# Optimization experiments

Hardware: AMD Instinct MI355X
Metric: run time of the kernel (lower is better)

Reference implementation:

```python
import jax, jax.numpy as jnp
import numpy as np

SCALE = 100.0
ALPHA_MEM = 0.9
ALPHA_MEM_OUT = 0.9
ALPHA_R = 0.85
ALPHA_X = 0.95
ALPHA_P = 0.95
ALPHA_D = 0.95
WMIN = 0.0
WMAX = 2.0


@jax.custom_vjp
def spike_fn(x):
    # SurrGradSpike.forward: heaviside(x)
    return (x > 0).astype(x.dtype)

def _spike_fwd(x):
    return spike_fn(x), x

def _spike_bwd(x, g):
    # SurrGradSpike.backward: g / (scale*|x| + 1)^2
    return (g / (SCALE * jnp.abs(x) + 1.0) ** 2,)

spike_fn.defvjp(_spike_fwd, _spike_bwd)


def setup_inputs() -> dict:
    key = jax.random.key(0)
    ks = jax.random.split(key, 8)
    B, T, NI, N, NO, D = 8, 64, 256, 512, 32, 4
    inputs = jax.random.normal(ks[0], (B, T, NI), jnp.float32)
    w = jax.random.normal(ks[1], (N, N), jnp.float32) * (0.1 / np.sqrt(N))
    w_in = jax.random.normal(ks[2], (NI, N), jnp.float32) * (1.0 / np.sqrt(NI))
    w_out = jax.random.normal(ks[3], (N, NO), jnp.float32) * (1.0 / np.sqrt(N))
    # each synapse (e,o) assigned exactly one delay bin -> one-hot delay map (D,N,N)
    delay_idx = jax.random.randint(ks[4], (N, N), 0, D)
    dmap = jax.nn.one_hot(delay_idx, D, axis=0, dtype=jnp.float32)
    delays = jnp.array([1, 2, 3, 5], jnp.int32)
    w_signs = jnp.where(jnp.arange(N) < (4 * N) // 5, 1.0, -1.0).astype(jnp.float32)
    p = jax.random.uniform(ks[5], (N,), jnp.float32, minval=-0.5, maxval=0.5)
    A_p = jax.random.uniform(ks[6], (N, N), jnp.float32, minval=0.0, maxval=1e-3)
    A_d = jax.random.uniform(ks[7], (N, N), jnp.float32, minval=0.0, maxval=1e-3)
    return dict(inputs=inputs, w=w, w_in=w_in, w_out=w_out, dmap=dmap,
                delays=delays, w_signs=w_signs, p=p, A_p=A_p, A_d=A_d)


def _snn_forward(inputs, w, w_in, w_out, dmap, delays, w_signs, p, A_p, A_d):
    B, T, _ = inputs.shape
    N = w.shape[0]
    dt = inputs.dtype
    # epoch state
    inp = jnp.einsum('btc,cn->btn', inputs, w_in)          # (B,T,N)
    W = dmap * (w_signs[:, None] * jnp.abs(w))             # (D,N,N)
    p_depr = (p < 0).astype(dt)

    mem = jnp.zeros((B, N), dt)
    w_p = jnp.zeros((B, N), dt)
    x_bar = jnp.zeros((B, N), dt)
    u_pot = jnp.zeros((B, N), dt)
    u_dep = jnp.zeros((B, N), dt)
    w_stdp = jnp.ones((B, N, N), dt)
    rec_out = jnp.zeros((T, B, N), dt)
    rec_wp = jnp.zeros((T, B, N), dt)
    rec_xb = jnp.zeros((T, B, N), dt)

    def step(carry, xt):
        mem, w_p, x_bar, u_pot, u_dep, w_stdp, rec_out, rec_wp, rec_xb = carry
        t, inp_t = xt
        # mark_spikes + record_state (records pre-update values)
        spike = spike_fn(mem - 1.0)
        rec_out = rec_out.at[t].set(spike)
        rec_wp = rec_wp.at[t].set(w_p)
        rec_xb = rec_xb.at[t].set(x_bar)
        # delayed gathers; negative torch indices hit zero-initialized tail -> %T
        idx = (t - delays) % T
        out_del = jnp.take(rec_out, idx, axis=0)           # (D,B,N)
        wp_del = jnp.take(rec_wp, idx, axis=0)
        xb_del = jnp.take(rec_xb, idx, axis=0)
        # synaptic input
        syn_p = out_del * (1.0 + wp_del)
        syn = jnp.einsum('dbe,deo,beo->bo', syn_p, W, w_stdp)
        # STP
        dw_p = spike * p * (1.0 + p_depr * w_p)
        w_p = w_p * ALPHA_R + dw_p
        # STDP (uses pre-update u_dep/u_pot/mem)
        X = jnp.einsum('dbe,deo->beo', out_del, dmap)
        dW_dep = X * A_d[None] * jax.nn.relu(u_dep)[:, None, :]
        xbar_d = jnp.einsum('dbe,deo->beo', xb_del, dmap)
        dW_pot = xbar_d * A_p[None] * (jax.lax.stop_gradient(spike) * jax.nn.relu(u_pot))[:, None, :]
        x_bar = ALPHA_X * x_bar + (1.0 - ALPHA_X) * jax.lax.stop_gradient(spike)
        u_pot = ALPHA_P * u_pot + (1.0 - ALPHA_P) * mem
        u_dep = ALPHA_D * u_dep + (1.0 - ALPHA_D) * mem
        w_stdp = jnp.clip(w_stdp + dW_pot - dW_dep, WMIN, WMAX)
        # membrane integration with spike reset (detached)
        mem = ALPHA_MEM * mem + inp_t + syn - jax.lax.stop_gradient(spike)
        return (mem, w_p, x_bar, u_pot, u_dep, w_stdp, rec_out, rec_wp, rec_xb), None

    carry = (mem, w_p, x_bar, u_pot, u_dep, w_stdp, rec_out, rec_wp, rec_xb)
    xs = (jnp.arange(T), jnp.swapaxes(inp, 0, 1))
    carry, _ = jax.lax.scan(jax.checkpoint(step), carry, xs)
    rec_out = carry[6]                                     # (T,B,N)
    # readout: leaky integrator over projected spikes
    h2 = jnp.einsum('btn,no->bto', jnp.swapaxes(rec_out, 0, 1), w_out)

    def ro_step(o, h):
        o = ALPHA_MEM_OUT * o + h
        return o, o

    _, readout = jax.lax.scan(ro_step, jnp.zeros((B, h2.shape[-1]), dt),
                              jnp.swapaxes(h2, 0, 1))
    return jnp.swapaxes(readout, 0, 1)                     # (B,T,n_outputs)


def reference(inputs, w, w_in, w_out, dmap, delays, w_signs, p, A_p, A_d):
    return _snn_forward(inputs, w, w_in, w_out, dmap, delays, w_signs, p, A_p, A_d)
```

## Files before the change

kernel.cpp:

```cpp
#include <hip/hip_runtime.h>
#include <stdint.h>


#define B  8
#define T  64
#define NI 256
#define NN 512
#define NO 32
#define DD 4

#define NBLK 256
#define TPB  256
#define OPB  16
#define SPL  32
#define EPAD 516
#define PLANE (DD*EPAD)

#define REC_ELEMS (T*B*NN)

__device__ __forceinline__ unsigned long long rec_load(const unsigned long long* p) {
    return __hip_atomic_load(p, __ATOMIC_RELAXED, __HIP_MEMORY_SCOPE_AGENT);
}
__device__ __forceinline__ void rec_store(unsigned long long* p, unsigned long long v) {
    __hip_atomic_store(p, v, __ATOMIC_RELAXED, __HIP_MEMORY_SCOPE_AGENT);
}
__device__ __forceinline__ bool is_sentinel(unsigned long long v) {
    return (unsigned int)(v >> 32) == 0xFFFFFFFFu;
}
__device__ __forceinline__ float2 unpack_rec(unsigned long long v) {
    return make_float2(__uint_as_float((unsigned int)v),
                       __uint_as_float((unsigned int)(v >> 32)));
}

__global__ __launch_bounds__(TPB, 1)
void snn_main(const float* __restrict__ inputs,
              const float* __restrict__ w,
              const float* __restrict__ w_in,
              const float* __restrict__ dmap,
              const int*   __restrict__ delays,
              const float* __restrict__ w_signs,
              const float* __restrict__ p,
              const float* __restrict__ A_p,
              const float* __restrict__ A_d,
              const float* __restrict__ w_out,
              unsigned long long* __restrict__ rec,
              float* __restrict__ out)
{
    __shared__ float2 sxq[2*PLANE];
    __shared__ float  inp_s[T*OPB];
    __shared__ float  hist[T][OPB];

    const int tid     = threadIdx.x;
    const int bid     = blockIdx.x;
    const int b       = bid & 7;
    const int chunk   = bid >> 3;
    const int o_base  = chunk * OPB;
    const int lane    = tid & 63;
    const int wave    = tid >> 6;
    const int e_grp   = lane >> 2;
    const int o_local = wave*4 + (lane & 3);
    const int o       = o_base + o_local;
    const bool pub    = (e_grp == 0);

    if (tid < OPB) rec_store(rec + (size_t)(0*B + b)*NN + o_base + tid, 0ull);

    float wv[SPL], ap[SPL], ad[SPL], ws[SPL];
    int   laddr[SPL];
    #pragma unroll
    for (int i = 0; i < SPL; ++i) {
        const int e = e_grp + 16*i;
        wv[i] = w_signs[e] * fabsf(w[e*NN + o]);
        ap[i] = A_p[e*NN + o];
        ad[i] = A_d[e*NN + o];
        int d = 0;
        if (dmap[1*NN*NN + e*NN + o] != 0.0f) d = 1;
        if (dmap[2*NN*NN + e*NN + o] != 0.0f) d = 2;
        if (dmap[3*NN*NN + e*NN + o] != 0.0f) d = 3;
        ws[i]    = 1.0f;
        laddr[i] = (d*EPAD + e) * 8;
    }
    int del[DD];
    #pragma unroll
    for (int d = 0; d < DD; ++d) del[d] = delays[d];

    {
        float* win = (float*)sxq;
        for (int k = tid; k < NI*OPB; k += TPB) {
            const int c = k >> 4, oo = k & 15;
            win[c*OPB + oo] = w_in[c*NN + o_base + oo];
        }
        __syncthreads();
        const int prow = tid >> 4, pcol = tid & 15;
        #pragma unroll
        for (int j = 0; j < 4; ++j) {
            const int tj = prow*4 + j;
            const float* inrow = inputs + (size_t)(b*T + tj)*NI;
            float a = 0.f;
            for (int c = 0; c < NI; ++c) a += inrow[c] * win[c*OPB + pcol];
            inp_s[tj*OPB + pcol] = a;
        }
        __syncthreads();
    }

    #pragma unroll
    for (int d = 0; d < DD; ++d) {
        sxq[d*EPAD + tid]       = make_float2(0.f, 0.f);
        sxq[d*EPAD + 256 + tid] = make_float2(0.f, 0.f);
    }
    __syncthreads();

    float mem = 0.f, w_p = 0.f, x_bar = 0.f, u_pot = 0.f, u_dep = 0.f;
    const float p_o  = p[o];
    const float pd_o = (p_o < 0.f) ? 1.f : 0.f;

    unsigned long long pk = 0ull;
    unsigned long long pf[DD][2];

    for (int t = 0; t < T; ++t) {
        if (t >= 1 && pub)
            rec_store(rec + (size_t)(t*B + b)*NN + o, pk);

        if (t + 1 < T) {
            #pragma unroll
            for (int d = 0; d < DD; ++d) {
                if (del[d] > 1 && t + 1 >= del[d]) {
                    const int s = (t + 1 - del[d]) & 63;
                    const unsigned long long* src = rec + (size_t)(s*B + b)*NN + tid;
                    pf[d][0] = rec_load(src);
                    pf[d][1] = rec_load(src + 256);
                }
            }
        }

        const float spike = (mem > 1.0f) ? 1.0f : 0.0f;
        if (pub) hist[t][o_local] = spike;
        const float pg  = spike * fmaxf(u_pot, 0.f);
        const float udr = fmaxf(u_dep, 0.f);

        const char* cbuf = (const char*)sxq + (t & 1)*(PLANE*8);
        float acc = 0.f;
        #pragma unroll
        for (int i = 0; i < SPL; ++i) {
            const float2 v = *(const float2*)(cbuf + laddr[i]);
            acc = fmaf(v.x, wv[i]*ws[i], acc);
            const unsigned int xu = __float_as_uint(v.y);
            const float dep = ((int)xu < 0) ? ad[i]*udr : 0.f;
            const float pot = (ap[i]*pg) * fabsf(v.y);
            ws[i] = fminf(fmaxf(ws[i] + pot - dep, 0.f), 2.f);
        }

        unsigned long long q0 = 0ull, q1 = 0ull;
        if (t + 1 < T) {
            #pragma unroll
            for (int d = 0; d < DD; ++d) {
                if (del[d] == 1) {
                    const unsigned long long* src = rec + (size_t)(t*B + b)*NN + tid;
                    q0 = rec_load(src);
                    q1 = rec_load(src + 256);
                }
            }
        }

        float a2 = acc + __shfl_xor(acc, 4);
        a2 += __shfl_xor(a2, 8);
        const int src0 = lane & 15;
        const float p0 = __shfl(a2, src0);
        const float p1 = __shfl(a2, src0 + 16);
        const float p2 = __shfl(a2, src0 + 32);
        const float p3 = __shfl(a2, src0 + 48);
        const float syn = ((p0 + p1) + p2) + p3;

        const float wp_new = 0.85f*w_p + spike * p_o * (1.f + pd_o*w_p);
        const float xb_new = 0.95f*x_bar + 0.05f*spike;
        u_pot = 0.95f*u_pot + 0.05f*mem;
        u_dep = 0.95f*u_dep + 0.05f*mem;
        mem   = 0.9f*mem + inp_s[t*OPB + o_local] + syn - spike;
        w_p   = wp_new;
        x_bar = xb_new;
        if (t + 1 < T) {
            const float spike1 = (mem > 1.0f) ? 1.0f : 0.0f;
            const float sp = spike1 * (1.f + w_p);
            const unsigned int xu = __float_as_uint(x_bar) | (spike1 != 0.f ? 0x80000000u : 0u);
            pk = ((unsigned long long)xu << 32) | (unsigned int)__float_as_uint(sp);
        }

        if (t + 1 < T) {
            float2* wbuf = sxq + ((t+1) & 1)*PLANE;
            #pragma unroll
            for (int d = 0; d < DD; ++d) {
                unsigned long long v0 = 0ull, v1 = 0ull;
                if (t + 1 >= del[d]) {
                    const int s = (t + 1 - del[d]) & 63;
                    const unsigned long long* src = rec + (size_t)(s*B + b)*NN + tid;
                    if (del[d] == 1) { v0 = q0;       v1 = q1;       }
                    else             { v0 = pf[d][0]; v1 = pf[d][1]; }
                    int guard = 0;
                    while (is_sentinel(v0) || is_sentinel(v1)) {
                        __builtin_amdgcn_s_sleep(1);
                        if (is_sentinel(v0)) v0 = rec_load(src);
                        if (is_sentinel(v1)) v1 = rec_load(src + 256);
                        if (++guard > (1 << 24)) break;
                    }
                }
                wbuf[d*EPAD + tid]       = unpack_rec(v0);
                wbuf[d*EPAD + 256 + tid] = unpack_rec(v1);
            }
        }
        __syncthreads();
    }

    if (tid < NO) {
        float wo[OPB];
        #pragma unroll
        for (int j = 0; j < OPB; ++j) wo[j] = w_out[(o_base + j)*NO + tid];
        float st = 0.f;
        for (int t = 0; t < T; ++t) {
            float h = 0.f;
            #pragma unroll
            for (int j = 0; j < OPB; ++j) h = fmaf(hist[t][j], wo[j], h);
            st = 0.9f*st + h;
            atomicAdd(out + ((size_t)b*T + t)*NO + tid, st);
        }
    }
}

extern "C" void kernel_launch(void* const* d_in, const int* in_sizes, int n_in,
                              void* d_out, int out_size, void* d_ws, size_t ws_size,
                              hipStream_t stream)
{
    const float* inputs  = (const float*)d_in[0];
    const float* w       = (const float*)d_in[1];
    const float* w_in    = (const float*)d_in[2];
    const float* w_out   = (const float*)d_in[3];
    const float* dmap    = (const float*)d_in[4];
    const int*   delays  = (const int*)  d_in[5];
    const float* w_signs = (const float*)d_in[6];
    const float* p       = (const float*)d_in[7];
    const float* A_p     = (const float*)d_in[8];
    const float* A_d     = (const float*)d_in[9];

    unsigned long long* rec = (unsigned long long*)d_ws;
    float* out = (float*)d_out;

    hipMemsetAsync(rec, 0xFF, (size_t)REC_ELEMS*8, stream);
    hipMemsetAsync(out, 0, (size_t)B*T*NO*4, stream);

    hipLaunchKernelGGL(snn_main, dim3(NBLK), dim3(TPB), 0, stream,
                       inputs, w, w_in, dmap, delays, w_signs, p, A_p, A_d,
                       w_out, rec, out);
}
```

Baseline: 278.3 us.

## Split work over 512 blocks of 128 threads and publish spikes immediately

Halves the outputs per block (16 to 8) and doubles the grid, so each thread stages four synapse rows instead of two and per-block recurrent work shrinks. The spike/trace record for step t+1 is now stored as soon as it is computed rather than deferred to the next iteration. The separate late load for delay-1 inputs is folded into the early prefetch. An early delay-1 load will usually see the sentinel and fall into the sleep-poll loop, and more blocks take part in the cross-block handshake each step.

```diff
diff --git a/kernel.cpp b/kernel.cpp
--- a/kernel.cpp
+++ b/kernel.cpp
@@ -9,9 +9,9 @@
 #define NO 32
 #define DD 4
 
-#define NBLK 256
-#define TPB  256
-#define OPB  16
+#define NBLK 512
+#define TPB  128
+#define OPB  8
 #define SPL  32
 #define EPAD 516
 #define PLANE (DD*EPAD)
@@ -86,11 +86,11 @@
     {
         float* win = (float*)sxq;
         for (int k = tid; k < NI*OPB; k += TPB) {
-            const int c = k >> 4, oo = k & 15;
+            const int c = k >> 3, oo = k & 7;
             win[c*OPB + oo] = w_in[c*NN + o_base + oo];
         }
         __syncthreads();
-        const int prow = tid >> 4, pcol = tid & 15;
+        const int prow = tid >> 3, pcol = tid & 7;
         #pragma unroll
         for (int j = 0; j < 4; ++j) {
             const int tj = prow*4 + j;
@@ -103,31 +103,27 @@
     }
 
     #pragma unroll
-    for (int d = 0; d < DD; ++d) {
-        sxq[d*EPAD + tid]       = make_float2(0.f, 0.f);
-        sxq[d*EPAD + 256 + tid] = make_float2(0.f, 0.f);
-    }
+    for (int d = 0; d < DD; ++d)
+        #pragma unroll
+        for (int k = 0; k < 4; ++k)
+            sxq[d*EPAD + k*TPB + tid] = make_float2(0.f, 0.f);
     __syncthreads();
 
     float mem = 0.f, w_p = 0.f, x_bar = 0.f, u_pot = 0.f, u_dep = 0.f;
     const float p_o  = p[o];
     const float pd_o = (p_o < 0.f) ? 1.f : 0.f;
 
-    unsigned long long pk = 0ull;
-    unsigned long long pf[DD][2];
+    unsigned long long pf[DD][4];
 
     for (int t = 0; t < T; ++t) {
-        if (t >= 1 && pub)
-            rec_store(rec + (size_t)(t*B + b)*NN + o, pk);
-
         if (t + 1 < T) {
             #pragma unroll
             for (int d = 0; d < DD; ++d) {
-                if (del[d] > 1 && t + 1 >= del[d]) {
+                if (t + 1 >= del[d]) {
                     const int s = (t + 1 - del[d]) & 63;
                     const unsigned long long* src = rec + (size_t)(s*B + b)*NN + tid;
-                    pf[d][0] = rec_load(src);
-                    pf[d][1] = rec_load(src + 256);
+                    #pragma unroll
+                    for (int k = 0; k < 4; ++k) pf[d][k] = rec_load(src + k*TPB);
                 }
             }
         }
@@ -147,18 +143,6 @@
             const float dep = ((int)xu < 0) ? ad[i]*udr : 0.f;
             const float pot = (ap[i]*pg) * fabsf(v.y);
             ws[i] = fminf(fmaxf(ws[i] + pot - dep, 0.f), 2.f);
-        }
-
-        unsigned long long q0 = 0ull, q1 = 0ull;
-        if (t + 1 < T) {
-            #pragma unroll
-            for (int d = 0; d < DD; ++d) {
-                if (del[d] == 1) {
-                    const unsigned long long* src = rec + (size_t)(t*B + b)*NN + tid;
-                    q0 = rec_load(src);
-                    q1 = rec_load(src + 256);
-                }
-            }
         }
 
         float a2 = acc + __shfl_xor(acc, 4);
@@ -177,33 +161,38 @@
         mem   = 0.9f*mem + inp_s[t*OPB + o_local] + syn - spike;
         w_p   = wp_new;
         x_bar = xb_new;
-        if (t + 1 < T) {
+
+        if (t + 1 < T && pub) {
             const float spike1 = (mem > 1.0f) ? 1.0f : 0.0f;
             const float sp = spike1 * (1.f + w_p);
             const unsigned int xu = __float_as_uint(x_bar) | (spike1 != 0.f ? 0x80000000u : 0u);
-            pk = ((unsigned long long)xu << 32) | (unsigned int)__float_as_uint(sp);
+            rec_store(rec + (size_t)((t+1)*B + b)*NN + o,
+                      ((unsigned long long)xu << 32) | (unsigned int)__float_as_uint(sp));
         }
 
         if (t + 1 < T) {
             float2* wbuf = sxq + ((t+1) & 1)*PLANE;
             #pragma unroll
             for (int d = 0; d < DD; ++d) {
-                unsigned long long v0 = 0ull, v1 = 0ull;
                 if (t + 1 >= del[d]) {
                     const int s = (t + 1 - del[d]) & 63;
                     const unsigned long long* src = rec + (size_t)(s*B + b)*NN + tid;
-                    if (del[d] == 1) { v0 = q0;       v1 = q1;       }
-                    else             { v0 = pf[d][0]; v1 = pf[d][1]; }
-                    int guard = 0;
-                    while (is_sentinel(v0) || is_sentinel(v1)) {
-                        __builtin_amdgcn_s_sleep(1);
-                        if (is_sentinel(v0)) v0 = rec_load(src);
-                        if (is_sentinel(v1)) v1 = rec_load(src + 256);
-                        if (++guard > (1 << 24)) break;
+                    #pragma unroll
+                    for (int k = 0; k < 4; ++k) {
+                        unsigned long long v = pf[d][k];
+                        int guard = 0;
+                        while (is_sentinel(v)) {
+                            __builtin_amdgcn_s_sleep(1);
+                            v = rec_load(src + k*TPB);
+                            if (++guard > (1 << 24)) break;
+                        }
+                        wbuf[d*EPAD + k*TPB + tid] = unpack_rec(v);
                     }
+                } else {
+                    #pragma unroll
+                    for (int k = 0; k < 4; ++k)
+                        wbuf[d*EPAD + k*TPB + tid] = make_float2(0.f, 0.f);
                 }
-                wbuf[d*EPAD + tid]       = unpack_rec(v0);
-                wbuf[d*EPAD + 256 + tid] = unpack_rec(v1);
             }
         }
         __syncthreads();
```

After: 338.4 us. 1.22x slower.
